# Performance work log

Hardware: AMD Instinct MI355X
Metric: run time of the kernel (lower is better)

Reference implementation:

```python
import jax, jax.numpy as jnp
import numpy as np
from jax import lax

DW_THR = 4.0
PW_THR = 1e-3
EPS = 1e-5


def _bn(x, gamma, beta, mean, var):
    # inference-mode BatchNorm2d over channel axis 1
    inv = gamma * lax.rsqrt(var + EPS)
    return x * inv[None, :, None, None] + (beta - mean * inv)[None, :, None, None]


def _prune(x, thr):
    # zero each (batch, channel) feature map whose max-abs < thr
    maxabs = jnp.max(jnp.abs(x), axis=(2, 3), keepdims=True)  # [B,C,1,1]
    return jnp.where(maxabs < thr, jnp.zeros((), x.dtype), x)


def setup_inputs() -> dict:
    key = jax.random.key(0)
    ks = jax.random.split(key, 8)
    B, Cin, Cout, H, W = 32, 256, 512, 56, 56
    x = jax.random.normal(ks[0], (B, Cin, H, W), jnp.float32)
    dw_w = jax.random.normal(ks[1], (Cin, 1, 3, 3), jnp.float32) * (1.0 / 3.0)
    dw_b = jax.random.normal(ks[2], (Cin,), jnp.float32) * 0.1
    bn1_gamma = jnp.ones((Cin,), jnp.float32)
    bn1_beta = jnp.zeros((Cin,), jnp.float32)
    bn1_mean = jnp.zeros((Cin,), jnp.float32)
    bn1_var = jnp.ones((Cin,), jnp.float32)
    pw_w = jax.random.normal(ks[3], (Cout, Cin), jnp.float32) * (1.0 / np.sqrt(Cin))
    pw_b = jax.random.normal(ks[4], (Cout,), jnp.float32) * 0.1
    bn2_gamma = jnp.ones((Cout,), jnp.float32)
    bn2_beta = jnp.zeros((Cout,), jnp.float32)
    bn2_mean = jnp.zeros((Cout,), jnp.float32)
    bn2_var = jnp.ones((Cout,), jnp.float32)
    return dict(x=x, dw_w=dw_w, dw_b=dw_b,
                bn1_gamma=bn1_gamma, bn1_beta=bn1_beta, bn1_mean=bn1_mean, bn1_var=bn1_var,
                pw_w=pw_w, pw_b=pw_b,
                bn2_gamma=bn2_gamma, bn2_beta=bn2_beta, bn2_mean=bn2_mean, bn2_var=bn2_var)


def reference(x, dw_w, dw_b, bn1_gamma, bn1_beta, bn1_mean, bn1_var,
              pw_w, pw_b, bn2_gamma, bn2_beta, bn2_mean, bn2_var):
    Cin = x.shape[1]
    # depthwise 3x3 conv, padding=1, groups=Cin
    y = lax.conv_general_dilated(
        x, dw_w, window_strides=(1, 1), padding=((1, 1), (1, 1)),
        feature_group_count=Cin,
        dimension_numbers=('NCHW', 'OIHW', 'NCHW'))
    y = y + dw_b[None, :, None, None]
    y = jax.nn.relu(_bn(y, bn1_gamma, bn1_beta, bn1_mean, bn1_var))
    y = _prune(y, DW_THR)
    # pointwise 1x1 conv == channel GEMM
    z = jnp.einsum('bchw,oc->bohw', y, pw_w) + pw_b[None, :, None, None]
    z = jax.nn.relu(_bn(z, bn2_gamma, bn2_beta, bn2_mean, bn2_var))
    z = _prune(z, PW_THR)
    return z
```

## Files before the change

### kernel.cpp

```cpp
#include <hip/hip_runtime.h>
#include <hip/hip_bf16.h>

#define EPSV 1e-5f
#define DW_THR 4.0f
#define PW_THR 1e-3f

static constexpr int BB = 32, CIN = 256, COUT = 512, HH = 56, WW = 56, HW = HH * WW;

typedef __attribute__((ext_vector_type(8))) short bf16x8;
typedef __attribute__((ext_vector_type(4))) float f32x4;
typedef __attribute__((ext_vector_type(8))) unsigned short u16x8;

__device__ __forceinline__ void glds16(const void* g, void* l) {
    __builtin_amdgcn_global_load_lds((const __attribute__((address_space(1))) void*)g,
                                     (__attribute__((address_space(3))) void*)l, 16, 0, 0);
}

__global__ __launch_bounds__(256) void dwfold_kernel(
    const float* __restrict__ x, const float* __restrict__ dw_w, const float* __restrict__ dw_b,
    const float* __restrict__ g1, const float* __restrict__ b1,
    const float* __restrict__ m1, const float* __restrict__ v1,
    const float* __restrict__ pw_w, const float* __restrict__ pw_b,
    const float* __restrict__ g2, const float* __restrict__ b2,
    const float* __restrict__ m2, const float* __restrict__ v2,
    __hip_bfloat16* __restrict__ y, int* __restrict__ flags,
    __hip_bfloat16* __restrict__ Wf, float* __restrict__ cterm)
{
    __shared__ float xs[58 * 68];
    __shared__ float redw[4];
    const int tid = threadIdx.x;

    if (blockIdx.x < COUT) {
        const int o = blockIdx.x;
        const float inv = g2[o] * rsqrtf(v2[o] + EPSV);
        Wf[o * CIN + tid] = __float2bfloat16(pw_w[o * CIN + tid] * inv);
        if (tid == 0) cterm[o] = (pw_b[o] - m2[o]) * inv + b2[o];
        return;
    }

    const int blk = blockIdx.x - COUT;
    const int c   = blk & (CIN - 1);

    if (tid < 228) {
        int idx;
        if (tid < 58)       idx = 3 + tid;
        else if (tid < 116) idx = 57 * 68 + 3 + (tid - 58);
        else if (tid < 172) idx = (tid - 116 + 1) * 68 + 3;
        else                idx = (tid - 172 + 1) * 68 + 60;
        xs[idx] = 0.f;
    }
    const float* xp = x + (size_t)blk * HW;
    for (int i = tid; i < 56 * 14; i += 256) {
        int r = i / 14, q = i - r * 14;
        *(f32x4*)&xs[(r + 1) * 68 + 4 + q * 4] = *(const f32x4*)(xp + i * 4);
    }

    float w[9];
#pragma unroll
    for (int k = 0; k < 9; k++) w[k] = dw_w[c * 9 + k];
    const float inv = g1[c] * rsqrtf(v1[c] + EPSV);
    const float sh  = (dw_b[c] - m1[c]) * inv + b1[c];
    __syncthreads();

    float vals[14];
    float mx = 0.f;
    const int row = tid >> 2, strip = tid & 3;
    if (tid < 224) {
        const float* base = xs + row * 68 + strip * 14 + 4;
        float a0 = base[-1],       a1 = base[0];
        float b0 = base[68 - 1],   b1v = base[68];
        float c0 = base[136 - 1],  c1 = base[136];
#pragma unroll
        for (int i = 0; i < 14; i++) {
            const float a2 = base[i + 1];
            const float b2v = base[68 + i + 1];
            const float c2 = base[136 + i + 1];
            float s;
            s = a0 * w[0];
            s = fmaf(a1, w[1], s); s = fmaf(a2, w[2], s);
            s = fmaf(b0, w[3], s); s = fmaf(b1v, w[4], s); s = fmaf(b2v, w[5], s);
            s = fmaf(c0, w[6], s); s = fmaf(c1, w[7], s); s = fmaf(c2, w[8], s);
            const float val = fmaxf(fmaf(s, inv, sh), 0.f);
            vals[i] = val;
            mx = fmaxf(mx, val);
            a0 = a1; a1 = a2; b0 = b1v; b1v = b2v; c0 = c1; c1 = c2;
        }
    }

    for (int off = 32; off > 0; off >>= 1) mx = fmaxf(mx, __shfl_xor(mx, off));
    if ((tid & 63) == 0) redw[tid >> 6] = mx;
    __syncthreads();
    const float bmax = fmaxf(fmaxf(redw[0], redw[1]), fmaxf(redw[2], redw[3]));
    const int survive = (bmax >= DW_THR) ? 1 : 0;
    if (tid == 0) flags[blk] = survive;
    if (survive && tid < 224) {
        unsigned short* yp = (unsigned short*)(y + (size_t)blk * HW) + row * 56 + strip * 14;
#pragma unroll
        for (int i = 0; i < 7; i++) {
            ushort2 pk;
            pk.x = __bfloat16_as_ushort(__float2bfloat16(vals[2 * i]));
            pk.y = __bfloat16_as_ushort(__float2bfloat16(vals[2 * i + 1]));
            *(ushort2*)(yp + 2 * i) = pk;
        }
    }
}

__global__ __launch_bounds__(256) void gemm_kernel(
    const __hip_bfloat16* __restrict__ Wf_, const __hip_bfloat16* __restrict__ y_,
    const int* __restrict__ flags, const float* __restrict__ cterm,
    float* __restrict__ out)
{
    const int orig = blockIdx.x;
    const int blk  = (orig & 7) * 400 + (orig >> 3);
    const int b    = blk / 100;
    const int rem  = blk % 100;
    const int mt = rem / 25, nt = rem % 25;
    const int tid = threadIdx.x, l = tid & 63, wid = tid >> 6;
    const int wm = wid >> 1, wn = wid & 1;
    const int lr = l & 15, lk = l >> 4;
    const int o0 = mt * 128, n0 = nt * 128;

    __shared__ unsigned short Al[128 * 32];
    __shared__ unsigned short Bl[128 * 34];
    __shared__ int fl[CIN];

    fl[tid] = flags[b * CIN + tid];

    const short* W = (const short*)Wf_;
    const unsigned short* Y = (const unsigned short*)y_ + (size_t)b * CIN * HW;

    const int kch   = (((l & 3) ^ ((l >> 3) & 3)) << 3);
    const int rowA  = o0 + 32 * wid + (l >> 2);
    const short* asrc0 = W + (size_t)rowA * CIN + kch;
    const short* asrc1 = W + (size_t)(rowA + 16) * CIN + kch;

    const int cp = tid & 15, ng = tid >> 4;
    const int nB = n0 + ng * 8;
    const int nloc = ng * 8;

    f32x4 acc[4][4];
#pragma unroll
    for (int nr = 0; nr < 4; nr++)
#pragma unroll
        for (int mr = 0; mr < 4; mr++) acc[nr][mr] = (f32x4){0.f, 0.f, 0.f, 0.f};

    __syncthreads();

#pragma unroll
    for (int t = 0; t < 8; t++) {
        const int k0 = t * 32;
        glds16(asrc0 + k0, (void*)(&Al[(2 * wid) * 512]));
        glds16(asrc1 + k0, (void*)(&Al[(2 * wid + 1) * 512]));

        const int c0 = k0 + cp * 2;
        u16x8 v0 = (u16x8){0,0,0,0,0,0,0,0}, v1 = (u16x8){0,0,0,0,0,0,0,0};
        if (fl[c0])     v0 = *(const u16x8*)(Y + (size_t)c0 * HW + nB);
        if (fl[c0 + 1]) v1 = *(const u16x8*)(Y + (size_t)(c0 + 1) * HW + nB);
#pragma unroll
        for (int j = 0; j < 8; j++) {
            const unsigned pk = (unsigned)v0[j] | ((unsigned)v1[j] << 16);
            *(unsigned*)((char*)Bl + (nloc + j) * 68 + cp * 4) = pk;
        }
        __syncthreads();

        bf16x8 a[4], bb[4];
#pragma unroll
        for (int mr = 0; mr < 4; mr++) {
            const int r = wm * 64 + mr * 16 + lr;
            a[mr] = *(const bf16x8*)((const char*)Al + r * 64 + ((lk ^ ((r >> 1) & 3)) << 4));
        }
#pragma unroll
        for (int nr = 0; nr < 4; nr++) {
            const int r = wn * 64 + nr * 16 + lr;
            bb[nr] = *(const bf16x8*)((const char*)Bl + r * 68 + lk * 16);
        }
#pragma unroll
        for (int nr = 0; nr < 4; nr++)
#pragma unroll
            for (int mr = 0; mr < 4; mr++)
                acc[nr][mr] = __builtin_amdgcn_mfma_f32_16x16x32_bf16(bb[nr], a[mr], acc[nr][mr], 0, 0, 0);
        __syncthreads();
    }

    float ct[4];
#pragma unroll
    for (int mr = 0; mr < 4; mr++) ct[mr] = cterm[o0 + wm * 64 + mr * 16 + lr];
    const int nb0 = n0 + wn * 64;
#pragma unroll
    for (int nr = 0; nr < 4; nr++) {
        const int n4 = nb0 + nr * 16 + lk * 4;
        if (n4 < HW) {
#pragma unroll
            for (int mr = 0; mr < 4; mr++) {
                const int o = o0 + wm * 64 + mr * 16 + lr;
                f32x4 z;
                z[0] = fmaxf(acc[nr][mr][0] + ct[mr], 0.f);
                z[1] = fmaxf(acc[nr][mr][1] + ct[mr], 0.f);
                z[2] = fmaxf(acc[nr][mr][2] + ct[mr], 0.f);
                z[3] = fmaxf(acc[nr][mr][3] + ct[mr], 0.f);
                __builtin_nontemporal_store(z, (f32x4*)(out + ((size_t)b * COUT + o) * HW + n4));
            }
        }
    }
}

extern "C" void kernel_launch(void* const* d_in, const int* in_sizes, int n_in,
                              void* d_out, int out_size, void* d_ws, size_t ws_size,
                              hipStream_t stream)
{
    const float* x    = (const float*)d_in[0];
    const float* dw_w = (const float*)d_in[1];
    const float* dw_b = (const float*)d_in[2];
    const float* g1   = (const float*)d_in[3];
    const float* b1   = (const float*)d_in[4];
    const float* m1   = (const float*)d_in[5];
    const float* v1   = (const float*)d_in[6];
    const float* pw_w = (const float*)d_in[7];
    const float* pw_b = (const float*)d_in[8];
    const float* g2   = (const float*)d_in[9];
    const float* b2   = (const float*)d_in[10];
    const float* m2   = (const float*)d_in[11];
    const float* v2   = (const float*)d_in[12];
    float* out = (float*)d_out;

    char* ws = (char*)d_ws;
    size_t off = 0;
    __hip_bfloat16* y  = (__hip_bfloat16*)(ws + off); off += (size_t)BB * CIN * HW * 2 + 256;
    int*   flags = (int*)(ws + off);   off += (size_t)BB * CIN * 4;
    __hip_bfloat16* Wf = (__hip_bfloat16*)(ws + off); off += (size_t)COUT * CIN * 2;
    float* cterm = (float*)(ws + off); off += (size_t)COUT * 4;

    dwfold_kernel<<<COUT + BB * CIN, 256, 0, stream>>>(
        x, dw_w, dw_b, g1, b1, m1, v1, pw_w, pw_b, g2, b2, m2, v2, y, flags, Wf, cterm);
    gemm_kernel<<<BB * 4 * 25, 256, 0, stream>>>(Wf, y, flags, cterm, out);
}
```

Baseline: 98.20 us.

## Double-buffer GEMM LDS tiles and batch weight folding into fewer blocks

The GEMM now keeps two LDS buffers for the A and B tiles. It issues the loads for the next K-step before running the MFMAs on the current one, so global-memory latency can overlap with compute. The weight-folding part of the first kernel now handles 8 output rows per block, cutting that grid section from 512 blocks to 64. Double buffering doubles the LDS footprint, which may reduce occupancy, and it depends on the barrier at the end of each loop iteration to avoid overwriting a buffer that is still being read.

```diff
diff --git a/kernel.cpp b/kernel.cpp
--- a/kernel.cpp
+++ b/kernel.cpp
@@ -30,15 +30,19 @@
     __shared__ float redw[4];
     const int tid = threadIdx.x;
 
-    if (blockIdx.x < COUT) {
-        const int o = blockIdx.x;
-        const float inv = g2[o] * rsqrtf(v2[o] + EPSV);
-        Wf[o * CIN + tid] = __float2bfloat16(pw_w[o * CIN + tid] * inv);
-        if (tid == 0) cterm[o] = (pw_b[o] - m2[o]) * inv + b2[o];
+    if (blockIdx.x < 64) {
+        const int ob = blockIdx.x * 8;
+#pragma unroll
+        for (int q = 0; q < 8; q++) {
+            const int o = ob + q;
+            const float inv = g2[o] * rsqrtf(v2[o] + EPSV);
+            Wf[o * CIN + tid] = __float2bfloat16(pw_w[o * CIN + tid] * inv);
+            if (tid == 0) cterm[o] = (pw_b[o] - m2[o]) * inv + b2[o];
+        }
         return;
     }
 
-    const int blk = blockIdx.x - COUT;
+    const int blk = blockIdx.x - 64;
     const int c   = blk & (CIN - 1);
 
     if (tid < 228) {
@@ -120,8 +124,8 @@
     const int lr = l & 15, lk = l >> 4;
     const int o0 = mt * 128, n0 = nt * 128;
 
-    __shared__ unsigned short Al[128 * 32];
-    __shared__ unsigned short Bl[128 * 34];
+    __shared__ unsigned short Al[2][128 * 32];
+    __shared__ unsigned short Bl[2][128 * 34];
     __shared__ int fl[CIN];
 
     fl[tid] = flags[b * CIN + tid];
@@ -144,14 +148,10 @@
 #pragma unroll
         for (int mr = 0; mr < 4; mr++) acc[nr][mr] = (f32x4){0.f, 0.f, 0.f, 0.f};
 
-    __syncthreads();
-
-#pragma unroll
-    for (int t = 0; t < 8; t++) {
+    auto STAGE = [&](int t, int s) {
         const int k0 = t * 32;
-        glds16(asrc0 + k0, (void*)(&Al[(2 * wid) * 512]));
-        glds16(asrc1 + k0, (void*)(&Al[(2 * wid + 1) * 512]));
-
+        glds16(asrc0 + k0, (void*)(&Al[s][(2 * wid) * 512]));
+        glds16(asrc1 + k0, (void*)(&Al[s][(2 * wid + 1) * 512]));
         const int c0 = k0 + cp * 2;
         u16x8 v0 = (u16x8){0,0,0,0,0,0,0,0}, v1 = (u16x8){0,0,0,0,0,0,0,0};
         if (fl[c0])     v0 = *(const u16x8*)(Y + (size_t)c0 * HW + nB);
@@ -159,20 +159,30 @@
 #pragma unroll
         for (int j = 0; j < 8; j++) {
             const unsigned pk = (unsigned)v0[j] | ((unsigned)v1[j] << 16);
-            *(unsigned*)((char*)Bl + (nloc + j) * 68 + cp * 4) = pk;
-        }
-        __syncthreads();
-
+            *(unsigned*)((char*)Bl[s] + (nloc + j) * 68 + cp * 4) = pk;
+        }
+    };
+
+    __syncthreads();
+    STAGE(0, 0);
+    __syncthreads();
+
+#pragma unroll
+    for (int t = 0; t < 8; t++) {
+        if (t < 7) STAGE(t + 1, (t + 1) & 1);
+
+        const char* alu = (const char*)Al[t & 1];
+        const char* blu = (const char*)Bl[t & 1];
         bf16x8 a[4], bb[4];
 #pragma unroll
         for (int mr = 0; mr < 4; mr++) {
             const int r = wm * 64 + mr * 16 + lr;
-            a[mr] = *(const bf16x8*)((const char*)Al + r * 64 + ((lk ^ ((r >> 1) & 3)) << 4));
+            a[mr] = *(const bf16x8*)(alu + r * 64 + ((lk ^ ((r >> 1) & 3)) << 4));
         }
 #pragma unroll
         for (int nr = 0; nr < 4; nr++) {
             const int r = wn * 64 + nr * 16 + lr;
-            bb[nr] = *(const bf16x8*)((const char*)Bl + r * 68 + lk * 16);
+            bb[nr] = *(const bf16x8*)(blu + r * 68 + lk * 16);
         }
 #pragma unroll
         for (int nr = 0; nr < 4; nr++)
@@ -230,7 +240,7 @@
     __hip_bfloat16* Wf = (__hip_bfloat16*)(ws + off); off += (size_t)COUT * CIN * 2;
     float* cterm = (float*)(ws + off); off += (size_t)COUT * 4;
 
-    dwfold_kernel<<<COUT + BB * CIN, 256, 0, stream>>>(
+    dwfold_kernel<<<64 + BB * CIN, 256, 0, stream>>>(
         x, dw_w, dw_b, g1, b1, m1, v1, pw_w, pw_b, g2, b2, m2, v2, y, flags, Wf, cterm);
     gemm_kernel<<<BB * 4 * 25, 256, 0, stream>>>(Wf, y, flags, cterm, out);
 }
```

Result: slower. 114.0 us (+16.1%).
